# Kernel tuning notes

Measured on AMD Instinct MI355X. Metric: run time of the kernel, lower is better.

The kernel has to match this reference:

```python
import jax, jax.numpy as jnp
import numpy as np
from jax import lax

NUM_HEADS = 3
HEAD_CH = 64  # in_ch // num_heads = 192 // 3
EPS = 1e-5   # haiku BatchNorm default eps


def _conv_proj(x, dw, scale, offset, pw, stride):
    # DepthwiseConv2D (SAME, no bias) -> BatchNorm (training: batch stats) -> 1x1 Conv (no bias)
    C = x.shape[-1]
    x = lax.conv_general_dilated(
        x, dw, (stride, stride), 'SAME',
        dimension_numbers=('NHWC', 'HWIO', 'NHWC'),
        feature_group_count=C)
    mean = x.mean(axis=(0, 1, 2))
    var = x.var(axis=(0, 1, 2))
    x = (x - mean) * lax.rsqrt(var + EPS) * scale + offset
    return jnp.einsum('bhwc,cd->bhwd', x, pw)  # pointwise 1x1 conv


def _split_heads(x):
    # b H W (h d) -> b h (H W) d
    b, hh, ww, c = x.shape
    return x.reshape(b, hh * ww, NUM_HEADS, HEAD_CH).transpose(0, 2, 1, 3)


def setup_inputs() -> dict:
    key = jax.random.key(0)
    ks = jax.random.split(key, 18)
    B, H, W, C = 16, 56, 56, 192
    Cout = NUM_HEADS * HEAD_CH  # 192
    g = lambda k, shape, s=0.02: jax.random.normal(k, shape, jnp.float32) * s
    return {
        'inputs_q':  jax.random.normal(ks[0], (B, H, W, C), jnp.float32),
        'inputs_kv': jax.random.normal(ks[1], (B, H, W, C), jnp.float32),
        # depthwise kernels (k, k, 1, C)
        'dw_q': g(ks[2], (3, 3, 1, C)), 'dw_k': g(ks[3], (3, 3, 1, C)), 'dw_v': g(ks[4], (3, 3, 1, C)),
        # BN scale/offset per projection
        'scale_q': jnp.ones((C,), jnp.float32), 'offset_q': jnp.zeros((C,), jnp.float32),
        'scale_k': jnp.ones((C,), jnp.float32), 'offset_k': jnp.zeros((C,), jnp.float32),
        'scale_v': jnp.ones((C,), jnp.float32), 'offset_v': jnp.zeros((C,), jnp.float32),
        # pointwise 1x1 conv kernels (C, Cout)
        'pw_q': g(ks[5], (C, Cout)), 'pw_k': g(ks[6], (C, Cout)), 'pw_v': g(ks[7], (C, Cout)),
        # talking-heads mixing matrices (h, h), near-identity init
        'pre_sm':  jnp.eye(NUM_HEADS, dtype=jnp.float32) + g(ks[8], (NUM_HEADS, NUM_HEADS), 0.1),
        'post_sm': jnp.eye(NUM_HEADS, dtype=jnp.float32) + g(ks[9], (NUM_HEADS, NUM_HEADS), 0.1),
        # output linear (no bias)
        'w_out': g(ks[10], (Cout, C)),
    }


def reference(inputs_q, inputs_kv, dw_q, dw_k, dw_v,
              scale_q, offset_q, scale_k, offset_k, scale_v, offset_v,
              pw_q, pw_k, pw_v, pre_sm, post_sm, w_out):
    q = _conv_proj(inputs_q,  dw_q, scale_q, offset_q, pw_q, 1)  # [B,56,56,192]
    k = _conv_proj(inputs_kv, dw_k, scale_k, offset_k, pw_k, 2)  # [B,28,28,192]
    v = _conv_proj(inputs_kv, dw_v, scale_v, offset_v, pw_v, 2)
    B = q.shape[0]
    q = _split_heads(q) / jnp.sqrt(jnp.float32(HEAD_CH))  # [B,h,Lq,d]
    k = _split_heads(k)                                   # [B,h,Lk,d]
    v = _split_heads(v)
    w = jnp.einsum('bhld,bhkd->bhlk', q, k)               # [B,h,Lq,Lk]
    w = jnp.einsum('bhlk,hg->bglk', w, pre_sm)            # pre-softmax talking heads
    w = jax.nn.softmax(w, axis=-1)
    w = jnp.einsum('bhlk,hg->bglk', w, post_sm)           # post-softmax talking heads
    s = jnp.einsum('bhlk,bhkd->bhld', w, v)               # [B,h,Lq,d]
    s = s.transpose(0, 2, 1, 3).reshape(B, -1, NUM_HEADS * HEAD_CH)  # b l (h d)
    return s @ w_out                                      # [B,Lq,192]
```

## Files before the change

### kernel.cpp

```cpp
#include <hip/hip_runtime.h>

using short8 = __attribute__((ext_vector_type(8))) short;
using f32x4  = __attribute__((ext_vector_type(4))) float;

__device__ __forceinline__ short f2bf(float f){
  unsigned u = __float_as_uint(f);
  unsigned r = (u + 0x7FFFu + ((u >> 16) & 1u)) >> 16;
  return (short)r;
}
__device__ __forceinline__ float sget(float x){
  return __uint_as_float(__builtin_amdgcn_readfirstlane(__float_as_uint(x)));
}
__device__ __forceinline__ void async_cp16(short* lds, const short* g){
  __builtin_amdgcn_global_load_lds((const __attribute__((address_space(1))) unsigned int*)g,
                                   (__attribute__((address_space(3))) unsigned int*)lds,
                                   16, 0, 0);
}

__global__ __launch_bounds__(384) void k_dw(const float* __restrict__ inq, const float* __restrict__ inkv,
                                            const float* __restrict__ wq, const float* __restrict__ wk,
                                            const float* __restrict__ wv,
                                            short* __restrict__ dqb, short* __restrict__ dkb,
                                            short* __restrict__ dvb, float2* __restrict__ partq,
                                            float2* __restrict__ partk, float2* __restrict__ partv){
  __shared__ float red[4][384];
  int t = threadIdx.x;
  int c = t % 192, strip = t / 192;
  if(blockIdx.x < 896){
    int bid = blockIdx.x; int b = bid / 56, oh = bid % 56;
    float w[9];
#pragma unroll
    for(int i=0;i<9;i++) w[i] = wq[i*192 + c];
    const float* inb = inq + (size_t)b*56*56*192;
    const float* rp[3]; bool rv[3];
#pragma unroll
    for(int kh=0;kh<3;kh++){
      int ih = oh + kh - 1;
      rv[kh] = (ih >= 0 && ih < 56);
      rp[kh] = inb + (size_t)(rv[kh] ? ih : 0)*56*192 + c;
    }
    auto ldc = [&](int kh, int iw)->float{
      return (rv[kh] && iw >= 0 && iw < 56) ? rp[kh][iw*192] : 0.f;
    };
    int ow0 = strip*28;
    float x0[3], x1[3];
#pragma unroll
    for(int kh=0;kh<3;kh++){ x0[kh] = ldc(kh, ow0-1); x1[kh] = ldc(kh, ow0); }
    float lsum = 0.f, lsq = 0.f;
    size_t orow = ((size_t)b*3136 + (size_t)oh*56)*192;
#pragma unroll 1
    for(int j=0;j<28;j++){
      int ow = ow0 + j;
      float x2[3];
#pragma unroll
      for(int kh=0;kh<3;kh++) x2[kh] = ldc(kh, ow+1);
      float acc = 0.f;
#pragma unroll
      for(int kh=0;kh<3;kh++){
        acc = fmaf(x0[kh], w[kh*3+0], acc);
        acc = fmaf(x1[kh], w[kh*3+1], acc);
        acc = fmaf(x2[kh], w[kh*3+2], acc);
      }
      dqb[orow + (size_t)ow*192 + c] = f2bf(acc);
      lsum += acc; lsq = fmaf(acc, acc, lsq);
#pragma unroll
      for(int kh=0;kh<3;kh++){ x0[kh] = x1[kh]; x1[kh] = x2[kh]; }
    }
    red[0][t] = lsum; red[1][t] = lsq;
    __syncthreads();
    if(t < 192){
      float2 o; o.x = lsum + red[0][t+192]; o.y = lsq + red[1][t+192];
      partq[(size_t)bid*192 + t] = o;
    }
  } else {
    int bid = blockIdx.x - 896; int b = bid / 28, oh = bid % 28;
    float wkr[9], wvr[9];
#pragma unroll
    for(int i=0;i<9;i++){ wkr[i] = wk[i*192 + c]; wvr[i] = wv[i*192 + c]; }
    const float* inb = inkv + (size_t)b*56*56*192;
    const float* rp[3]; bool rv[3];
#pragma unroll
    for(int kh=0;kh<3;kh++){
      int ih = 2*oh + kh;
      rv[kh] = (ih < 56);
      rp[kh] = inb + (size_t)(rv[kh] ? ih : 0)*56*192 + c;
    }
    auto ldc = [&](int kh, int iw)->float{
      return (rv[kh] && iw < 56) ? rp[kh][iw*192] : 0.f;
    };
    int ow0 = strip*14;
    float xp[3];
#pragma unroll
    for(int kh=0;kh<3;kh++) xp[kh] = ldc(kh, 2*ow0);
    float ksum=0.f, ksq=0.f, vsum=0.f, vsq=0.f;
    size_t orow = ((size_t)b*784 + (size_t)oh*28)*192;
#pragma unroll 1
    for(int j=0;j<14;j++){
      int ow = ow0 + j;
      float xm[3], xn[3];
#pragma unroll
      for(int kh=0;kh<3;kh++){ xm[kh] = ldc(kh, 2*ow+1); xn[kh] = ldc(kh, 2*ow+2); }
      float ak = 0.f, av = 0.f;
#pragma unroll
      for(int kh=0;kh<3;kh++){
        ak = fmaf(xp[kh], wkr[kh*3+0], ak); ak = fmaf(xm[kh], wkr[kh*3+1], ak); ak = fmaf(xn[kh], wkr[kh*3+2], ak);
        av = fmaf(xp[kh], wvr[kh*3+0], av); av = fmaf(xm[kh], wvr[kh*3+1], av); av = fmaf(xn[kh], wvr[kh*3+2], av);
      }
      dkb[orow + (size_t)ow*192 + c] = f2bf(ak);
      dvb[orow + (size_t)ow*192 + c] = f2bf(av);
      ksum += ak; ksq = fmaf(ak, ak, ksq);
      vsum += av; vsq = fmaf(av, av, vsq);
#pragma unroll
      for(int kh=0;kh<3;kh++) xp[kh] = xn[kh];
    }
    red[0][t]=ksum; red[1][t]=ksq; red[2][t]=vsum; red[3][t]=vsq;
    __syncthreads();
    if(t < 192){
      float2 a; a.x = ksum + red[0][t+192]; a.y = ksq + red[1][t+192];
      partk[(size_t)bid*192 + t] = a;
      float2 o; o.x = vsum + red[2][t+192]; o.y = vsq + red[3][t+192];
      partv[(size_t)bid*192 + t] = o;
    }
  }
}

__global__ __launch_bounds__(192) void k_red(const float2* __restrict__ pq, const float2* __restrict__ pk,
                                             const float2* __restrict__ pv, float2* __restrict__ oq,
                                             float2* __restrict__ ok2, float2* __restrict__ ov2){
  int blk = blockIdx.x, t = threadIdx.x;
  const float2* src; float2* dst;
  if(blk < 8){ src = pq + (size_t)blk*112*192;      dst = oq  + (size_t)blk*192; }
  else if(blk < 12){ src = pk + (size_t)(blk-8)*112*192;  dst = ok2 + (size_t)(blk-8)*192; }
  else { src = pv + (size_t)(blk-12)*112*192; dst = ov2 + (size_t)(blk-12)*192; }
  float s=0.f, q=0.f;
#pragma unroll 8
  for(int i=0;i<112;i++){ float2 v = src[(size_t)i*192 + t]; s += v.x; q += v.y; }
  float2 o; o.x=s; o.y=q; dst[t] = o;
}

__global__ __launch_bounds__(192) void k_fin(const float2* __restrict__ pq, const float2* __restrict__ pk,
                                             const float2* __restrict__ pv,
                                             const float* __restrict__ sq, const float* __restrict__ oq,
                                             const float* __restrict__ sk, const float* __restrict__ ok,
                                             const float* __restrict__ sv, const float* __restrict__ ov,
                                             const float* __restrict__ pwq, const float* __restrict__ pwk,
                                             const float* __restrict__ pwv, const float* __restrict__ wout,
                                             short* __restrict__ Wt, float* __restrict__ bias){
  int p = blockIdx.x, t = threadIdx.x;
  __shared__ float aS[192], bS[192];
  if(p < 3){
    const float2* part = (p==0)?pq:((p==1)?pk:pv);
    int nb = (p==0)?8:4;
    float N = (p==0)?50176.f:12544.f;
    const float* sc = (p==0)?sq:((p==1)?sk:sv);
    const float* of = (p==0)?oq:((p==1)?ok:ov);
    float s=0.f, q2=0.f;
#pragma unroll
    for(int i=0;i<8;i++){ if(i<nb){ float2 v = part[(size_t)i*192 + t]; s += v.x; q2 += v.y; } }
    float mean = s / N;
    float var  = q2 / N - mean*mean;
    float a  = rsqrtf(var + 1e-5f) * sc[t];
    float bv = of[t] - mean*a;
    aS[t] = a; bS[t] = bv;
    __syncthreads();
    const float* pw = (p==0)?pwq:((p==1)?pwk:pwv);
    float qs = (p==0) ? 0.125f : 1.0f;
    float bacc = 0.f;
    for(int cc=0; cc<192; cc++){
      float wv_ = pw[cc*192 + t];
      bacc = fmaf(bS[cc], wv_, bacc);
      Wt[((size_t)p*192 + t)*192 + cc] = f2bf(aS[cc]*wv_*qs);
    }
    bias[p*192 + t] = bacc * qs;
  } else {
    for(int cc=0; cc<192; cc++) Wt[((size_t)3*192 + t)*192 + cc] = f2bf(wout[cc*192 + t]);
    bias[3*192 + t] = 0.f;
  }
}

__global__ __launch_bounds__(256) void k_kv(const short* __restrict__ dkb, const short* __restrict__ dvb,
                                            const short* __restrict__ Wt, const float* __restrict__ bias,
                                            short* __restrict__ kbuf, short* __restrict__ vtb){
  int blk = blockIdx.x;
  bool isV = blk >= 208;
  int pb = isV ? blk - 208 : blk;
  int w = threadIdx.x >> 6, L = threadIdx.x & 63, l16 = L & 15, h4 = L >> 4;
  int row0 = pb*64 + w*16;
  int b = row0 / 832, kk0 = row0 - b*832;
  const short* A = isV ? dvb : dkb;
  const short* Wp = Wt + (isV ? 2 : 1)*36864;
  const float* bp = bias + (isV ? 2 : 1)*192;
  int kkA = kk0 + l16; if(kkA > 783) kkA = 783;
  short8 af[6];
  const short8* arow = (const short8*)(A + (size_t)(b*784 + kkA)*192);
#pragma unroll
  for(int kf=0;kf<6;kf++) af[kf] = arow[kf*4 + h4];
  short* obase = (isV ? vtb : kbuf) + (size_t)b*26*6144;
#pragma unroll
  for(int nt=0;nt<12;nt++){
    f32x4 acc = f32x4{0.f,0.f,0.f,0.f};
    const short8* wrow = (const short8*)(Wp + (size_t)(nt*16 + l16)*192);
#pragma unroll
    for(int kf=0;kf<6;kf++)
      acc = __builtin_amdgcn_mfma_f32_16x16x32_bf16(af[kf], wrow[kf*4 + h4], acc, 0,0,0);
    int col = nt*16 + l16;
    float bv = bp[col];
#pragma unroll
    for(int r=0;r<4;r++){
      int kk = kk0 + h4*4 + r;
      float v = (kk < 784) ? (acc[r] + bv) : 0.f;
      int t = kk >> 5, rr = kk & 31;
      if(!isV) obase[(size_t)t*6144 + (col>>3)*256 + rr*8 + (col&7)] = f2bf(v);
      else     obase[(size_t)t*6144 + (rr>>3)*1536 + col*8 + (rr&7)] = f2bf(v);
    }
  }
}

__global__ __launch_bounds__(256, 4) void k_attn(const short* __restrict__ dq, const short* __restrict__ Wt,
                                                 const float* __restrict__ bias,
                                                 const short* __restrict__ kb, const short* __restrict__ vt,
                                                 const float* __restrict__ pre, const float* __restrict__ post,
                                                 float* __restrict__ outp){
  __shared__ __align__(16) short sS[19968];
  short* sK0 = sS;
  short* sK1 = sS + 6144;
  short* sP  = sS + 12288;
  int bid = blockIdx.x;
  int b  = ((bid & 7) << 1) | ((bid >> 3) & 1);
  int lt = bid >> 4;
  int tid = threadIdx.x; int w = tid >> 6, lane = tid & 63, l16 = lane & 15, h4 = lane >> 4;
  int lw = lt*64 + w*16;
  short* sScr = sS + w*3200;

  {
    short8 af[6];
    const short8* arow = (const short8*)(dq + ((size_t)b*3136 + lw + l16)*192);
#pragma unroll
    for(int kf=0;kf<6;kf++) af[kf] = arow[kf*4 + h4];
#pragma unroll
    for(int nt=0;nt<12;nt++){
      f32x4 acc = f32x4{0.f,0.f,0.f,0.f};
      const short8* wrow = (const short8*)(Wt + (size_t)(nt*16 + l16)*192);
#pragma unroll
      for(int kf=0;kf<6;kf++)
        acc = __builtin_amdgcn_mfma_f32_16x16x32_bf16(af[kf], wrow[kf*4 + h4], acc, 0,0,0);
      float bv = bias[nt*16 + l16];
#pragma unroll
      for(int r=0;r<4;r++) sScr[(h4*4+r)*200 + nt*16 + l16] = f2bf(acc[r] + bv);
    }
  }
  short8 qf[3][2];
#pragma unroll
  for(int h=0;h<3;h++)
#pragma unroll
    for(int kf=0;kf<2;kf++) qf[h][kf] = *(const short8*)&sScr[l16*200 + h*64 + kf*32 + h4*8];

  float pm[3][3];
#pragma unroll
  for(int h=0;h<3;h++)
#pragma unroll
    for(int g=0;g<3;g++) pm[h][g] = sget(pre[h*3+g]);

  const short* kgb = kb + (size_t)b*26*6144;
  const short* vgb = vt + (size_t)b*26*6144;
  int soff = w*1536;

  auto stageK = [&](int t, int pb_){
    const short* kg = kgb + (size_t)t*6144 + soff + lane*8;
    short* kl = (pb_ ? sK1 : sK0) + soff;
#pragma unroll
    for(int j=0;j<3;j++) async_cp16(kl + j*512, kg + j*512);
  };

  float Zp[3][4];
#pragma unroll
  for(int g=0;g<3;g++)
#pragma unroll
    for(int r=0;r<4;r++) Zp[g][r] = 0.f;

  __syncthreads();
  stageK(0, 0);
  __syncthreads();

#pragma unroll 1
  for(int ks=0; ks<25; ks++){
    if(ks < 24) stageK(ks+1, (ks+1)&1);
    const short* sKc = (ks&1) ? sK1 : sK0;
#pragma unroll
    for(int nt=0;nt<2;nt++){
      f32x4 a3[3];
#pragma unroll
      for(int h=0;h<3;h++) a3[h] = f32x4{0.f,0.f,0.f,0.f};
#pragma unroll
      for(int h=0;h<3;h++)
#pragma unroll
        for(int kf=0;kf<2;kf++){
          short8 bk = *(const short8*)&sKc[(h*8 + kf*4 + h4)*256 + (nt*16 + l16)*8];
          a3[h] = __builtin_amdgcn_mfma_f32_16x16x32_bf16(qf[h][kf], bk, a3[h], 0,0,0);
        }
      bool valid = (ks*32 + nt*16 + l16) < 784;
#pragma unroll
      for(int r=0;r<4;r++){
        float s0 = a3[0][r], s1 = a3[1][r], s2 = a3[2][r];
#pragma unroll
        for(int g=0;g<3;g++){
          float sm = fmaf(pm[0][g], s0, fmaf(pm[1][g], s1, pm[2][g]*s2));
          Zp[g][r] += valid ? __expf(sm) : 0.f;
        }
      }
    }
    __syncthreads();
  }

  float invZ[3][4];
#pragma unroll
  for(int g=0;g<3;g++)
#pragma unroll
    for(int r=0;r<4;r++){
      float z = Zp[g][r];
      z += __shfl_xor(z, 1); z += __shfl_xor(z, 2); z += __shfl_xor(z, 4); z += __shfl_xor(z, 8);
      invZ[g][r] = 1.f / z;
    }
  float po[3][3];
#pragma unroll
  for(int g=0;g<3;g++)
#pragma unroll
    for(int gp=0;gp<3;gp++) po[g][gp] = sget(post[g*3+gp]);

  f32x4 U[3][4];
#pragma unroll
  for(int gp=0;gp<3;gp++)
#pragma unroll
    for(int nt=0;nt<4;nt++) U[gp][nt] = f32x4{0.f,0.f,0.f,0.f};

  stageK(0, 0);
  __syncthreads();

  int sPw = w*1920;
#pragma unroll 1
  for(int ks=0; ks<25; ks++){
    if(ks < 24) stageK(ks+1, (ks+1)&1);
    const short* sKc = (ks&1) ? sK1 : sK0;
#pragma unroll
    for(int nt=0;nt<2;nt++){
      f32x4 a3[3];
#pragma unroll
      for(int h=0;h<3;h++) a3[h] = f32x4{0.f,0.f,0.f,0.f};
#pragma unroll
      for(int h=0;h<3;h++)
#pragma unroll
        for(int kf=0;kf<2;kf++){
          short8 bk = *(const short8*)&sKc[(h*8 + kf*4 + h4)*256 + (nt*16 + l16)*8];
          a3[h] = __builtin_amdgcn_mfma_f32_16x16x32_bf16(qf[h][kf], bk, a3[h], 0,0,0);
        }
      bool valid = (ks*32 + nt*16 + l16) < 784;
#pragma unroll
      for(int r=0;r<4;r++){
        float s0 = a3[0][r], s1 = a3[1][r], s2 = a3[2][r];
        float pn[3];
#pragma unroll
        for(int g=0;g<3;g++){
          float sm = fmaf(pm[0][g], s0, fmaf(pm[1][g], s1, pm[2][g]*s2));
          pn[g] = (valid ? __expf(sm) : 0.f) * invZ[g][r];
        }
#pragma unroll
        for(int gp=0;gp<3;gp++){
          float wp = fmaf(po[0][gp], pn[0], fmaf(po[1][gp], pn[1], po[2][gp]*pn[2]));
          sP[sPw + gp*640 + (h4*4+r)*40 + nt*16 + l16] = f2bf(wp);
        }
      }
    }
    const short* vtile = vgb + (size_t)ks*6144 + h4*1536;
#pragma unroll
    for(int gp=0;gp<3;gp++){
      short8 pa = *(const short8*)&sP[sPw + gp*640 + l16*40 + h4*8];
#pragma unroll
      for(int nt=0;nt<4;nt++){
        short8 vb = *(const short8*)(vtile + (gp*64 + nt*16 + l16)*8);
        U[gp][nt] = __builtin_amdgcn_mfma_f32_16x16x32_bf16(pa, vb, U[gp][nt], 0,0,0);
      }
    }
    __syncthreads();
  }

#pragma unroll
  for(int gp=0;gp<3;gp++)
#pragma unroll
    for(int nt=0;nt<4;nt++)
#pragma unroll
      for(int r=0;r<4;r++)
        sScr[(h4*4+r)*200 + gp*64 + nt*16 + l16] = f2bf(U[gp][nt][r]);
  short8 uf[6];
#pragma unroll
  for(int kf=0;kf<6;kf++) uf[kf] = *(const short8*)&sScr[l16*200 + kf*32 + h4*8];
  const short* W3 = Wt + 3*36864;
#pragma unroll
  for(int nt=0;nt<12;nt++){
    f32x4 acc = f32x4{0.f,0.f,0.f,0.f};
    const short8* wrow = (const short8*)(W3 + (size_t)(nt*16 + l16)*192);
#pragma unroll
    for(int kf=0;kf<6;kf++)
      acc = __builtin_amdgcn_mfma_f32_16x16x32_bf16(uf[kf], wrow[kf*4 + h4], acc, 0,0,0);
#pragma unroll
    for(int r=0;r<4;r++)
      outp[((size_t)b*3136 + lw + h4*4 + r)*192 + nt*16 + l16] = acc[r];
  }
}

extern "C" void kernel_launch(void* const* d_in, const int* in_sizes, int n_in,
                              void* d_out, int out_size, void* d_ws, size_t ws_size,
                              hipStream_t stream){
  (void)in_sizes; (void)n_in; (void)out_size; (void)ws_size;
  const float* inq  = (const float*)d_in[0];
  const float* inkv = (const float*)d_in[1];
  const float* dwq  = (const float*)d_in[2];
  const float* dwk  = (const float*)d_in[3];
  const float* dwv  = (const float*)d_in[4];
  const float* scq  = (const float*)d_in[5];  const float* ofq = (const float*)d_in[6];
  const float* sck  = (const float*)d_in[7];  const float* ofk = (const float*)d_in[8];
  const float* scv  = (const float*)d_in[9];  const float* ofv = (const float*)d_in[10];
  const float* pwq  = (const float*)d_in[11];
  const float* pwk  = (const float*)d_in[12];
  const float* pwv  = (const float*)d_in[13];
  const float* pre  = (const float*)d_in[14];
  const float* post = (const float*)d_in[15];
  const float* wout = (const float*)d_in[16];

  char* ws = (char*)d_ws;
  size_t off = 0;
  auto alloc = [&](size_t bytes)->void*{ void* p = ws + off; off += (bytes + 255) & ~(size_t)255; return p; };
  short*  dqb  = (short*) alloc(50176ull*192*2);
  short*  dkb  = (short*) alloc(12544ull*192*2);
  short*  dvb  = (short*) alloc(12544ull*192*2);
  short*  kbuf = (short*) alloc(16ull*26*6144*2);
  short*  vtb  = (short*) alloc(16ull*26*6144*2);
  float2* pq   = (float2*)alloc(896ull*192*sizeof(float2));
  float2* pk   = (float2*)alloc(448ull*192*sizeof(float2));
  float2* pv   = (float2*)alloc(448ull*192*sizeof(float2));
  float2* pq2  = (float2*)alloc(8ull*192*sizeof(float2));
  float2* pk2  = (float2*)alloc(4ull*192*sizeof(float2));
  float2* pv2  = (float2*)alloc(4ull*192*sizeof(float2));
  short*  Wt   = (short*) alloc(4ull*192*192*2);
  float*  bias = (float*) alloc(4ull*192*4);

  k_dw<<<1344, 384, 0, stream>>>(inq, inkv, dwq, dwk, dwv, dqb, dkb, dvb, pq, pk, pv);
  k_red<<<16, 192, 0, stream>>>(pq, pk, pv, pq2, pk2, pv2);
  k_fin<<<4, 192, 0, stream>>>(pq2, pk2, pv2, scq, ofq, sck, ofk, scv, ofv, pwq, pwk, pwv, wout, Wt, bias);
  k_kv<<<416, 256, 0, stream>>>(dkb, dvb, Wt, bias, kbuf, vtb);
  k_attn<<<784, 256, 0, stream>>>(dqb, Wt, bias, kbuf, vtb, pre, post, (float*)d_out);
}
```

Before: 290.3 us.

## Split softmax normalizer pass into separate kernel and use exp2 with packed bf16

Moves the first pass that computes softmax row sums out of the attention kernel into a new k_z kernel, which writes inverse normalizers to a global buffer. The attention kernel now only runs the probability and PV pass. Separately, log2(e) is folded into the Q projection scale so both kernels can call exp2f. The QK MFMA operands are swapped so each lane holds four consecutive key columns, which lets the bf16 stores be packed with v_cvt_pk_bf16. Costs: Q is recomputed in both kernels, there is an extra launch and global round trip, and occupancy on k_attn drops to 3. The padding masks for the PV pass are removed, so correctness relies on padded K/V rows holding zeros or bias.

```diff
diff --git a/kernel.cpp b/kernel.cpp
--- a/kernel.cpp
+++ b/kernel.cpp
@@ -10,6 +10,11 @@
 }
 __device__ __forceinline__ float sget(float x){
   return __uint_as_float(__builtin_amdgcn_readfirstlane(__float_as_uint(x)));
+}
+__device__ __forceinline__ unsigned cvtpk_bf16(float lo, float hi){
+  unsigned d;
+  asm("v_cvt_pk_bf16_f32 %0, %1, %2" : "=v"(d) : "v"(lo), "v"(hi));
+  return d;
 }
 __device__ __forceinline__ void async_cp16(short* lds, const short* g){
   __builtin_amdgcn_global_load_lds((const __attribute__((address_space(1))) unsigned int*)g,
@@ -164,7 +169,7 @@
     aS[t] = a; bS[t] = bv;
     __syncthreads();
     const float* pw = (p==0)?pwq:((p==1)?pwk:pwv);
-    float qs = (p==0) ? 0.125f : 1.0f;
+    float qs = (p==0) ? 0.125f*1.44269504f : 1.0f;
     float bacc = 0.f;
     for(int cc=0; cc<192; cc++){
       float wv_ = pw[cc*192 + t];
@@ -216,14 +221,105 @@
   }
 }
 
-__global__ __launch_bounds__(256, 4) void k_attn(const short* __restrict__ dq, const short* __restrict__ Wt,
+__global__ __launch_bounds__(256, 4) void k_z(const short* __restrict__ dq, const short* __restrict__ Wt,
+                                              const float* __restrict__ bias, const short* __restrict__ kb,
+                                              const float* __restrict__ pre, float* __restrict__ zb){
+  __shared__ __align__(16) short sS[12800];
+  short* sKb = sS;
+  int bid = blockIdx.x;
+  int b  = ((bid & 7) << 1) | ((bid >> 3) & 1);
+  int lt = bid >> 4;
+  int tid = threadIdx.x; int w = tid >> 6, lane = tid & 63, l16 = lane & 15, h4 = lane >> 4;
+  int lw = lt*64 + w*16;
+  short* sScr = sS + w*3200;
+
+  {
+    short8 af[6];
+    const short8* arow = (const short8*)(dq + ((size_t)b*3136 + lw + l16)*192);
+#pragma unroll
+    for(int kf=0;kf<6;kf++) af[kf] = arow[kf*4 + h4];
+#pragma unroll
+    for(int nt=0;nt<12;nt++){
+      f32x4 acc = f32x4{0.f,0.f,0.f,0.f};
+      const short8* wrow = (const short8*)(Wt + (size_t)(nt*16 + l16)*192);
+#pragma unroll
+      for(int kf=0;kf<6;kf++)
+        acc = __builtin_amdgcn_mfma_f32_16x16x32_bf16(af[kf], wrow[kf*4 + h4], acc, 0,0,0);
+      float bv = bias[nt*16 + l16];
+#pragma unroll
+      for(int r=0;r<4;r++) sScr[(h4*4+r)*200 + nt*16 + l16] = f2bf(acc[r] + bv);
+    }
+  }
+  short8 qf[3][2];
+#pragma unroll
+  for(int h=0;h<3;h++)
+#pragma unroll
+    for(int kf=0;kf<2;kf++) qf[h][kf] = *(const short8*)&sScr[l16*200 + h*64 + kf*32 + h4*8];
+
+  float pm[3][3];
+#pragma unroll
+  for(int h=0;h<3;h++)
+#pragma unroll
+    for(int g=0;g<3;g++) pm[h][g] = sget(pre[h*3+g]);
+
+  const short* kgb = kb + (size_t)b*26*6144;
+  int soff = w*1536;
+  auto stageK = [&](int t){
+    short* kl = sKb + (t&1)*6144 + soff;
+    const short* kg = kgb + (size_t)t*6144 + soff + lane*8;
+#pragma unroll
+    for(int j=0;j<3;j++) async_cp16(kl + j*512, kg + j*512);
+  };
+
+  float Zp[3] = {0.f, 0.f, 0.f};
+  __syncthreads();
+  stageK(0);
+  __syncthreads();
+
+#pragma unroll 1
+  for(int ks=0; ks<25; ks++){
+    if(ks < 24) stageK(ks+1);
+    const short* sKc = sKb + (ks&1)*6144;
+#pragma unroll
+    for(int nt=0;nt<2;nt++){
+      f32x4 a3[3];
+#pragma unroll
+      for(int h=0;h<3;h++) a3[h] = f32x4{0.f,0.f,0.f,0.f};
+#pragma unroll
+      for(int h=0;h<3;h++)
+#pragma unroll
+        for(int kf=0;kf<2;kf++){
+          short8 bk = *(const short8*)&sKc[(h*8 + kf*4 + h4)*256 + (nt*16 + l16)*8];
+          a3[h] = __builtin_amdgcn_mfma_f32_16x16x32_bf16(bk, qf[h][kf], a3[h], 0,0,0);
+        }
+      bool zok = (ks < 24) || (nt == 0);
+#pragma unroll
+      for(int g=0;g<3;g++){
+        float e0=0,e1=0,e2=0,e3=0;
+        e0 = exp2f(fmaf(pm[0][g], a3[0][0], fmaf(pm[1][g], a3[1][0], pm[2][g]*a3[2][0])));
+        e1 = exp2f(fmaf(pm[0][g], a3[0][1], fmaf(pm[1][g], a3[1][1], pm[2][g]*a3[2][1])));
+        e2 = exp2f(fmaf(pm[0][g], a3[0][2], fmaf(pm[1][g], a3[1][2], pm[2][g]*a3[2][2])));
+        e3 = exp2f(fmaf(pm[0][g], a3[0][3], fmaf(pm[1][g], a3[1][3], pm[2][g]*a3[2][3])));
+        if(zok) Zp[g] += (e0 + e1) + (e2 + e3);
+      }
+    }
+    __syncthreads();
+  }
+#pragma unroll
+  for(int g=0;g<3;g++){
+    float z = Zp[g];
+    z += __shfl_xor(z, 16); z += __shfl_xor(z, 32);
+    if(lane < 16) zb[((size_t)b*3 + g)*3136 + lw + l16] = 1.f / z;
+  }
+}
+
+__global__ __launch_bounds__(256, 3) void k_attn(const short* __restrict__ dq, const short* __restrict__ Wt,
                                                  const float* __restrict__ bias,
                                                  const short* __restrict__ kb, const short* __restrict__ vt,
                                                  const float* __restrict__ pre, const float* __restrict__ post,
-                                                 float* __restrict__ outp){
+                                                 const float* __restrict__ zb, float* __restrict__ outp){
   __shared__ __align__(16) short sS[19968];
-  short* sK0 = sS;
-  short* sK1 = sS + 6144;
+  short* sKb = sS;
   short* sP  = sS + 12288;
   int bid = blockIdx.x;
   int b  = ((bid & 7) << 1) | ((bid >> 3) & 1);
@@ -255,92 +351,41 @@
 #pragma unroll
     for(int kf=0;kf<2;kf++) qf[h][kf] = *(const short8*)&sScr[l16*200 + h*64 + kf*32 + h4*8];
 
-  float pm[3][3];
+  float pm[3][3], po[3][3];
 #pragma unroll
   for(int h=0;h<3;h++)
 #pragma unroll
-    for(int g=0;g<3;g++) pm[h][g] = sget(pre[h*3+g]);
+    for(int g=0;g<3;g++){ pm[h][g] = sget(pre[h*3+g]); po[h][g] = sget(post[h*3+g]); }
+
+  float izq[3];
+#pragma unroll
+  for(int g=0;g<3;g++) izq[g] = zb[((size_t)b*3 + g)*3136 + lw + l16];
+
+  f32x4 U[3][4];
+#pragma unroll
+  for(int gp=0;gp<3;gp++)
+#pragma unroll
+    for(int nt=0;nt<4;nt++) U[gp][nt] = f32x4{0.f,0.f,0.f,0.f};
 
   const short* kgb = kb + (size_t)b*26*6144;
   const short* vgb = vt + (size_t)b*26*6144;
   int soff = w*1536;
-
-  auto stageK = [&](int t, int pb_){
+  auto stageK = [&](int t){
+    short* kl = sKb + (t&1)*6144 + soff;
     const short* kg = kgb + (size_t)t*6144 + soff + lane*8;
-    short* kl = (pb_ ? sK1 : sK0) + soff;
 #pragma unroll
     for(int j=0;j<3;j++) async_cp16(kl + j*512, kg + j*512);
   };
 
-  float Zp[3][4];
-#pragma unroll
-  for(int g=0;g<3;g++)
-#pragma unroll
-    for(int r=0;r<4;r++) Zp[g][r] = 0.f;
-
   __syncthreads();
-  stageK(0, 0);
-  __syncthreads();
-
-#pragma unroll 1
-  for(int ks=0; ks<25; ks++){
-    if(ks < 24) stageK(ks+1, (ks+1)&1);
-    const short* sKc = (ks&1) ? sK1 : sK0;
-#pragma unroll
-    for(int nt=0;nt<2;nt++){
-      f32x4 a3[3];
-#pragma unroll
-      for(int h=0;h<3;h++) a3[h] = f32x4{0.f,0.f,0.f,0.f};
-#pragma unroll
-      for(int h=0;h<3;h++)
-#pragma unroll
-        for(int kf=0;kf<2;kf++){
-          short8 bk = *(const short8*)&sKc[(h*8 + kf*4 + h4)*256 + (nt*16 + l16)*8];
-          a3[h] = __builtin_amdgcn_mfma_f32_16x16x32_bf16(qf[h][kf], bk, a3[h], 0,0,0);
-        }
-      bool valid = (ks*32 + nt*16 + l16) < 784;
-#pragma unroll
-      for(int r=0;r<4;r++){
-        float s0 = a3[0][r], s1 = a3[1][r], s2 = a3[2][r];
-#pragma unroll
-        for(int g=0;g<3;g++){
-          float sm = fmaf(pm[0][g], s0, fmaf(pm[1][g], s1, pm[2][g]*s2));
-          Zp[g][r] += valid ? __expf(sm) : 0.f;
-        }
-      }
-    }
-    __syncthreads();
-  }
-
-  float invZ[3][4];
-#pragma unroll
-  for(int g=0;g<3;g++)
-#pragma unroll
-    for(int r=0;r<4;r++){
-      float z = Zp[g][r];
-      z += __shfl_xor(z, 1); z += __shfl_xor(z, 2); z += __shfl_xor(z, 4); z += __shfl_xor(z, 8);
-      invZ[g][r] = 1.f / z;
-    }
-  float po[3][3];
-#pragma unroll
-  for(int g=0;g<3;g++)
-#pragma unroll
-    for(int gp=0;gp<3;gp++) po[g][gp] = sget(post[g*3+gp]);
-
-  f32x4 U[3][4];
-#pragma unroll
-  for(int gp=0;gp<3;gp++)
-#pragma unroll
-    for(int nt=0;nt<4;nt++) U[gp][nt] = f32x4{0.f,0.f,0.f,0.f};
-
-  stageK(0, 0);
+  stageK(0);
   __syncthreads();
 
   int sPw = w*1920;
 #pragma unroll 1
   for(int ks=0; ks<25; ks++){
-    if(ks < 24) stageK(ks+1, (ks+1)&1);
-    const short* sKc = (ks&1) ? sK1 : sK0;
+    if(ks < 24) stageK(ks+1);
+    const short* sKc = sKb + (ks&1)*6144;
 #pragma unroll
     for(int nt=0;nt<2;nt++){
       f32x4 a3[3];
@@ -351,23 +396,24 @@
 #pragma unroll
         for(int kf=0;kf<2;kf++){
           short8 bk = *(const short8*)&sKc[(h*8 + kf*4 + h4)*256 + (nt*16 + l16)*8];
-          a3[h] = __builtin_amdgcn_mfma_f32_16x16x32_bf16(qf[h][kf], bk, a3[h], 0,0,0);
+          a3[h] = __builtin_amdgcn_mfma_f32_16x16x32_bf16(bk, qf[h][kf], a3[h], 0,0,0);
         }
-      bool valid = (ks*32 + nt*16 + l16) < 784;
-#pragma unroll
-      for(int r=0;r<4;r++){
-        float s0 = a3[0][r], s1 = a3[1][r], s2 = a3[2][r];
-        float pn[3];
-#pragma unroll
-        for(int g=0;g<3;g++){
-          float sm = fmaf(pm[0][g], s0, fmaf(pm[1][g], s1, pm[2][g]*s2));
-          pn[g] = (valid ? __expf(sm) : 0.f) * invZ[g][r];
+      float pn[3][4];
+#pragma unroll
+      for(int g=0;g<3;g++)
+#pragma unroll
+        for(int r=0;r<4;r++){
+          float sm = fmaf(pm[0][g], a3[0][r], fmaf(pm[1][g], a3[1][r], pm[2][g]*a3[2][r]));
+          pn[g][r] = exp2f(sm) * izq[g];
         }
 #pragma unroll
-        for(int gp=0;gp<3;gp++){
-          float wp = fmaf(po[0][gp], pn[0], fmaf(po[1][gp], pn[1], po[2][gp]*pn[2]));
-          sP[sPw + gp*640 + (h4*4+r)*40 + nt*16 + l16] = f2bf(wp);
-        }
+      for(int gp=0;gp<3;gp++){
+        float w0 = fmaf(po[0][gp], pn[0][0], fmaf(po[1][gp], pn[1][0], po[2][gp]*pn[2][0]));
+        float w1 = fmaf(po[0][gp], pn[0][1], fmaf(po[1][gp], pn[1][1], po[2][gp]*pn[2][1]));
+        float w2 = fmaf(po[0][gp], pn[0][2], fmaf(po[1][gp], pn[1][2], po[2][gp]*pn[2][2]));
+        float w3 = fmaf(po[0][gp], pn[0][3], fmaf(po[1][gp], pn[1][3], po[2][gp]*pn[2][3]));
+        uint2 dw; dw.x = cvtpk_bf16(w0, w1); dw.y = cvtpk_bf16(w2, w3);
+        *(uint2*)&sP[sPw + gp*640 + l16*40 + nt*16 + h4*4] = dw;
       }
     }
     const short* vtile = vgb + (size_t)ks*6144 + h4*1536;
@@ -434,6 +480,7 @@
   short*  dvb  = (short*) alloc(12544ull*192*2);
   short*  kbuf = (short*) alloc(16ull*26*6144*2);
   short*  vtb  = (short*) alloc(16ull*26*6144*2);
+  float*  zbuf = (float*) alloc(16ull*3*3136*4);
   float2* pq   = (float2*)alloc(896ull*192*sizeof(float2));
   float2* pk   = (float2*)alloc(448ull*192*sizeof(float2));
   float2* pv   = (float2*)alloc(448ull*192*sizeof(float2));
@@ -447,5 +494,6 @@
   k_red<<<16, 192, 0, stream>>>(pq, pk, pv, pq2, pk2, pv2);
   k_fin<<<4, 192, 0, stream>>>(pq2, pk2, pv2, scq, ofq, sck, ofk, scv, ofv, pwq, pwk, pwv, wout, Wt, bias);
   k_kv<<<416, 256, 0, stream>>>(dkb, dvb, Wt, bias, kbuf, vtb);
-  k_attn<<<784, 256, 0, stream>>>(dqb, Wt, bias, kbuf, vtb, pre, post, (float*)d_out);
-}
+  k_z<<<784, 256, 0, stream>>>(dqb, Wt, bias, kbuf, pre, zbuf);
+  k_attn<<<784, 256, 0, stream>>>(dqb, Wt, bias, kbuf, vtb, pre, post, zbuf, (float*)d_out);
+}
```

Result: slower. 446.4 us (+53.8%).
